# Kernel tuning notes

Hardware: AMD Instinct MI355X
Metric: run time of the kernel (lower is better)

## Reference

```python
import jax, jax.numpy as jnp
import numpy as np
from jax import lax

B, T, N, H, E = 128, 128, 49, 1024, 1024
EPS = 1e-6

def setup_inputs() -> dict:
    key = jax.random.key(0)
    ks = jax.random.split(key, 9)
    s = 0.02
    return {
        "X": jax.random.normal(ks[0], (B, T, E), jnp.float32),
        "G": jax.random.normal(ks[1], (2, B, H), jnp.float32),
        "L": jax.random.normal(ks[2], (B, N, H), jnp.float32),
        "W_ih0": jax.random.normal(ks[3], (3 * H, E), jnp.float32) * s,
        "W_hh0": jax.random.normal(ks[4], (3 * H, H), jnp.float32) * s,
        "W_ih1": jax.random.normal(ks[5], (3 * H, H), jnp.float32) * s,
        "W_hh1": jax.random.normal(ks[6], (3 * H, H), jnp.float32) * s,
        "W_lin": jax.random.normal(ks[7], (H, 2 * H), jnp.float32) * s,
        "a2": jnp.ones((H,), jnp.float32),
        "b2": jnp.zeros((H,), jnp.float32),
    }

def _gru_cell(x, h, W_ih, W_hh):
    # PyTorch GRUCell (bias=False): gates in order r, z, n
    gi = x @ W_ih.T  # [B, 3H]
    gh = h @ W_hh.T  # [B, 3H]
    i_r, i_z, i_n = jnp.split(gi, 3, axis=-1)
    h_r, h_z, h_n = jnp.split(gh, 3, axis=-1)
    r = jax.nn.sigmoid(i_r + h_r)
    z = jax.nn.sigmoid(i_z + h_z)
    n = jnp.tanh(i_n + r * h_n)
    return (1.0 - z) * n + z * h

def reference(X, G, L, W_ih0, W_hh0, W_ih1, W_hh1, W_lin, a2, b2):
    # NOTE: source attn() returns its input h (the bmm/softmax result is
    # discarded), so attention is dead code; dropout is eval-mode identity.
    def step(carry, xt):
        h0, h1_prev = carry            # each [B, H]
        h1 = _gru_cell(xt, h0, W_ih0, W_hh0)
        h2 = _gru_cell(h1, h1_prev, W_ih1, W_hh1)
        h_ = h2                        # drop (identity) + dead attn
        h0_new = jnp.tanh(jnp.concatenate([h0, h_], axis=1) @ W_lin.T)
        return (h0_new, h2), h0_new

    xs = jnp.swapaxes(X, 0, 1)         # [T, B, E]
    _, ys = lax.scan(step, (G[0], G[1]), xs)
    out = jnp.swapaxes(ys, 0, 1)       # [B, T, H]

    # LayerNorm with unbiased std and (std + eps) denominator (as in source)
    mean = out.mean(-1, keepdims=True)
    std = out.std(-1, ddof=1, keepdims=True)
    return a2 * (out - mean) / (std + EPS) + b2
```

## Files before the change

### kernel.cpp

```cpp
#include <hip/hip_runtime.h>
#include <hip/hip_bf16.h>

#define BB 128
#define TT 128
#define HH 1024
#define NWG 256
#define NT 512

typedef __bf16 bf16x8 __attribute__((ext_vector_type(8)));
typedef __bf16 bf16x4 __attribute__((ext_vector_type(4)));
typedef float  f32x4v __attribute__((ext_vector_type(4)));

#define MFMA16(a,b,c) __builtin_amdgcn_mfma_f32_16x16x32_bf16(a,b,c,0,0,0)

__device__ inline float fsig(float x) {
  x = fminf(fmaxf(x, -30.f), 30.f);
  return 1.f / (1.f + __expf(-x));
}
__device__ inline float ftanh(float x) {
  x = fminf(fmaxf(x, -15.f), 15.f);
  float e = __expf(2.f * x);
  return (e - 1.f) / (e + 1.f);
}
__device__ inline float bf2f(unsigned short u) {
  union { unsigned int i; float f; } c; c.i = (unsigned int)u << 16; return c.f;
}
__device__ inline void ucst16(__bf16* p, float v) {
  union { __bf16 b; unsigned short u; } c; c.b = (__bf16)v;
  __hip_atomic_store((unsigned short*)p, c.u, __ATOMIC_RELAXED, __HIP_MEMORY_SCOPE_AGENT);
}

#define SIGF(F) do { \
  __syncthreads(); \
  if (tid == 0) \
    __hip_atomic_store(&(F)[g], t + 1, __ATOMIC_RELAXED, __HIP_MEMORY_SCOPE_AGENT); \
} while (0)

__device__ inline void wf1(const int* F, int tgt, int tid, int lane) {
  if (tid < 64) {
    while (__hip_atomic_load(&F[lane], __ATOMIC_RELAXED, __HIP_MEMORY_SCOPE_AGENT) < tgt)
      __builtin_amdgcn_s_sleep(1);
    __builtin_amdgcn_fence(__ATOMIC_ACQUIRE, "agent");
  }
  __syncthreads();
  __builtin_amdgcn_sched_barrier(0);
}
__device__ inline void whalf(const int* F, int ch, int tgt, int tid, int lane) {
  if (tid < 64) {
    const int* P = F + ch * 32 + (lane & 31);
    while (__hip_atomic_load(P, __ATOMIC_RELAXED, __HIP_MEMORY_SCOPE_AGENT) < tgt)
      __builtin_amdgcn_s_sleep(1);
    __builtin_amdgcn_fence(__ATOMIC_ACQUIRE, "agent");
  }
  __syncthreads();
  __builtin_amdgcn_sched_barrier(0);
}

__device__ inline void stage_strip(char* dst, const float* src, int rstride, int tid) {
#pragma unroll
  for (int it = 0; it < 8; ++it) {
    int i = tid + it * NT;
    int rr = i >> 8;
    int c4 = i & 255;
    f32x4v v = *(const f32x4v*)(src + (size_t)rr * rstride + c4 * 4);
    bf16x4 o;
#pragma unroll
    for (int j = 0; j < 4; ++j) o[j] = (__bf16)v[j];
    *(bf16x4*)(dst + rr * 2048 + ((c4 * 8) ^ ((rr & 7) << 4))) = o;
  }
}

__device__ inline void stage_strip_b16(char* dst, const __bf16* src, int tid) {
#pragma unroll
  for (int it = 0; it < 8; ++it) {
    int i = tid + it * 256;
    int rr = i >> 7;
    int c8 = i & 127;
    bf16x8 v = *(const bf16x8*)(src + (size_t)rr * 1024 + c8 * 8);
    *(bf16x8*)(dst + rr * 2048 + ((c8 * 16) ^ ((rr & 7) << 4))) = v;
  }
}

template<int NS>
__device__ inline void gemm_half(const char* sm, const __bf16* __restrict__ A,
                                 int rowbase, int lane, int kb0, f32x4v (&acc)[NS]) {
  const int r = lane & 15, q = lane >> 4;
  const __bf16* Ap = A + (size_t)(rowbase + r) * 1024 + q * 8;
  bf16x8 a[16];
#pragma unroll
  for (int i = 0; i < 16; ++i) a[i] = *(const bf16x8*)(Ap + (kb0 + i) * 32);
  __builtin_amdgcn_sched_barrier(0);
  __builtin_amdgcn_s_setprio(1);
#pragma unroll
  for (int i = 0; i < 16; ++i) {
    const int kb = kb0 + i;
    const int byteo = (kb * 64 + q * 16) ^ ((r & 7) << 4);
#pragma unroll
    for (int s = 0; s < NS; ++s) {
      bf16x8 b = *(const bf16x8*)(sm + s * 32768 + r * 2048 + byteo);
      acc[s] = MFMA16(a[i], b, acc[s]);
    }
  }
  __builtin_amdgcn_s_setprio(0);
}

template<int NS>
__device__ inline void gemm_burst(const char* sm, const __bf16* __restrict__ A,
                                  int rowbase, int lane, f32x4v (&acc)[NS]) {
  const int r = lane & 15, q = lane >> 4;
  const __bf16* Ap = A + (size_t)(rowbase + r) * 1024 + q * 8;
  bf16x8 a[32];
#pragma unroll
  for (int kb = 0; kb < 32; ++kb) a[kb] = *(const bf16x8*)(Ap + kb * 32);
  __builtin_amdgcn_sched_barrier(0);
  __builtin_amdgcn_s_setprio(1);
#pragma unroll
  for (int kb = 0; kb < 32; ++kb) {
    const int byteo = (kb * 64 + q * 16) ^ ((r & 7) << 4);
#pragma unroll
    for (int s = 0; s < NS; ++s) {
      bf16x8 b = *(const bf16x8*)(sm + s * 32768 + r * 2048 + byteo);
      acc[s] = MFMA16(a[kb], b, acc[s]);
    }
  }
  __builtin_amdgcn_s_setprio(0);
}

__global__ void __launch_bounds__(NT, 2) gru_persist(
    const float* __restrict__ Whh0, const float* __restrict__ Wih1,
    const float* __restrict__ Whh1, const float* __restrict__ Wlin,
    const __bf16* __restrict__ gi0b, const float* __restrict__ G,
    __bf16* __restrict__ h0b, __bf16* __restrict__ h1b,
    __bf16* __restrict__ h2b, __bf16* __restrict__ gh1b,
    float* __restrict__ out, int* flags)
{
  __shared__ char sm[106496];
  float* h2s = (float*)(sm + 98304);
  const int tid = threadIdx.x, wg = blockIdx.x;
  const int wv = tid >> 6, lane = tid & 63;
  const int xcd = wg & 7;
  const int role = xcd >> 1;
  const int g = ((wg >> 3) << 1) | (xcd & 1);
  const int c0 = g * 16;
  const int r = lane & 15, q = lane >> 4;
  const bool gw = (wv < 4);

  if (role == 0) {
    stage_strip(sm,         Whh0 + (size_t)c0 * 1024,          1024, tid);
    stage_strip(sm + 32768, Whh0 + (size_t)(1024 + c0) * 1024, 1024, tid);
    stage_strip(sm + 65536, Whh0 + (size_t)(2048 + c0) * 1024, 1024, tid);
  } else if (role == 1) {
    stage_strip(sm,         Whh1 + (size_t)c0 * 1024,          1024, tid);
    stage_strip(sm + 32768, Whh1 + (size_t)(1024 + c0) * 1024, 1024, tid);
    stage_strip(sm + 65536, Whh1 + (size_t)(2048 + c0) * 1024, 1024, tid);
  } else if (role == 2) {
    stage_strip(sm,         Wih1 + (size_t)c0 * 1024,          1024, tid);
    stage_strip(sm + 32768, Wih1 + (size_t)(1024 + c0) * 1024, 1024, tid);
    stage_strip(sm + 65536, Wih1 + (size_t)(2048 + c0) * 1024, 1024, tid);
    for (int i = tid; i < 2048; i += NT) {
      int row = i >> 4, cc = i & 15;
      h2s[i] = G[131072 + row * 1024 + c0 + cc];
    }
  } else {
    stage_strip(sm,         Wlin + (size_t)c0 * 2048,        2048, tid);
    stage_strip(sm + 32768, Wlin + (size_t)c0 * 2048 + 1024, 2048, tid);
  }
  __syncthreads();

  int* F0h[2] = { flags + 0,   flags + 64 };
  int* F1h[2] = { flags + 128, flags + 192 };
  int* F2h[2] = { flags + 256, flags + 320 };
  int* F3h[2] = { flags + 384, flags + 448 };

  if (role == 0) {
    for (int t = 0; t < TT; ++t) {
      __bf16* h1bP = h1b + (size_t)(t & 1) * 131072;
#pragma unroll
      for (int h = 0; h < 2; ++h) {
        const int rowbase = h * 64 + wv * 16;
        f32x4v acc[3];
#pragma unroll
        for (int s = 0; s < 3; ++s) { f32x4v z = {0,0,0,0}; acc[s] = z; }
        whalf(F3h[h], 0, t, tid, lane);
        if (gw) gemm_half<3>(sm, h0b, rowbase, lane, 0, acc);
        whalf(F3h[h], 1, t, tid, lane);
        unsigned short ph[4], pgr[4], pgz[4], pgn[4];
        if (gw) {
#pragma unroll
          for (int gg = 0; gg < 4; ++gg) {
            int row = rowbase + q * 4 + gg;
            ph[gg] = *(const unsigned short*)(h0b + (size_t)row * 1024 + c0 + r);
            const unsigned short* gp =
                (const unsigned short*)(gi0b + ((size_t)t * 128 + row) * 3072 + c0 + r);
            pgr[gg] = gp[0]; pgz[gg] = gp[1024]; pgn[gg] = gp[2048];
          }
          gemm_half<3>(sm, h0b, rowbase, lane, 16, acc);
#pragma unroll
          for (int gg = 0; gg < 4; ++gg) {
            int row = rowbase + q * 4 + gg;
            float rv = fsig(bf2f(pgr[gg]) + acc[0][gg]);
            float zv = fsig(bf2f(pgz[gg]) + acc[1][gg]);
            float nv = ftanh(bf2f(pgn[gg]) + rv * acc[2][gg]);
            ucst16(h1bP + (size_t)row * 1024 + c0 + r, (1.f - zv) * nv + zv * bf2f(ph[gg]));
          }
        }
        SIGF(F0h[h]);
      }
    }
  } else if (role == 1) {
    for (int t = 0; t < TT; ++t) {
#pragma unroll
      for (int h = 0; h < 2; ++h) {
        wf1(F2h[h], t, tid, lane);
        if (gw) {
          const int rowbase = h * 64 + wv * 16;
          f32x4v acc[3];
#pragma unroll
          for (int s = 0; s < 3; ++s) { f32x4v z = {0,0,0,0}; acc[s] = z; }
          gemm_burst<3>(sm, h2b, rowbase, lane, acc);
#pragma unroll
          for (int gg = 0; gg < 4; ++gg) {
            size_t base = (size_t)(rowbase + q * 4 + gg) * 3072 + c0 + r;
            ucst16(gh1b + base,        acc[0][gg]);
            ucst16(gh1b + base + 1024, acc[1][gg]);
            ucst16(gh1b + base + 2048, acc[2][gg]);
          }
        }
        SIGF(F1h[h]);
      }
    }
  } else if (role == 2) {
    for (int t = 0; t < TT; ++t) {
      const __bf16* h1bP = h1b + (size_t)(t & 1) * 131072;
#pragma unroll
      for (int h = 0; h < 2; ++h) {
        const int rowbase = h * 64 + wv * 16;
        wf1(F1h[h], t + 1, tid, lane);
        unsigned short hg0[4], hg1[4], hg2[4];
        if (gw) {
#pragma unroll
          for (int gg = 0; gg < 4; ++gg) {
            int row = rowbase + q * 4 + gg;
            const unsigned short* hp = (const unsigned short*)(gh1b + (size_t)row * 3072 + c0 + r);
            hg0[gg] = hp[0]; hg1[gg] = hp[1024]; hg2[gg] = hp[2048];
          }
        }
        f32x4v acc[3];
#pragma unroll
        for (int s = 0; s < 3; ++s) { f32x4v z = {0,0,0,0}; acc[s] = z; }
        whalf(F0h[h], 0, t + 1, tid, lane);
        if (gw) gemm_half<3>(sm, h1bP, rowbase, lane, 0, acc);
        whalf(F0h[h], 1, t + 1, tid, lane);
        if (gw) {
          gemm_half<3>(sm, h1bP, rowbase, lane, 16, acc);
#pragma unroll
          for (int gg = 0; gg < 4; ++gg) {
            int row = rowbase + q * 4 + gg;
            float rv = fsig(acc[0][gg] + bf2f(hg0[gg]));
            float zv = fsig(acc[1][gg] + bf2f(hg1[gg]));
            float nv = ftanh(acc[2][gg] + rv * bf2f(hg2[gg]));
            float hp = h2s[row * 16 + r];
            float h2 = (1.f - zv) * nv + zv * hp;
            h2s[row * 16 + r] = h2;
            ucst16(h2b + (size_t)row * 1024 + c0 + r, h2);
          }
        }
        SIGF(F2h[h]);
      }
    }
  } else {
    for (int t = 0; t < TT; ++t) {
#pragma unroll
      for (int h = 0; h < 2; ++h) {
        const int rowbase = h * 64 + wv * 16;
        wf1(F3h[h], t, tid, lane);
        f32x4v accL[1];
        { f32x4v z = {0,0,0,0}; accL[0] = z; }
        if (gw) gemm_burst<1>(sm, h0b, rowbase, lane, accL);
        f32x4v accR[1];
        { f32x4v z = {0,0,0,0}; accR[0] = z; }
        whalf(F2h[h], 0, t + 1, tid, lane);
        if (gw) gemm_half<1>(sm + 32768, h2b, rowbase, lane, 0, accR);
        whalf(F2h[h], 1, t + 1, tid, lane);
        if (gw) {
          gemm_half<1>(sm + 32768, h2b, rowbase, lane, 16, accR);
#pragma unroll
          for (int gg = 0; gg < 4; ++gg) {
            int row = rowbase + q * 4 + gg;
            float v = ftanh(accL[0][gg] + accR[0][gg]);
            ucst16(h0b + (size_t)row * 1024 + c0 + r, v);
            out[((size_t)row * 128 + t) * 1024 + c0 + r] = v;
          }
        }
        SIGF(F3h[h]);
      }
    }
  }
}

__global__ void __launch_bounds__(256) gi0_kernel(const float* __restrict__ X,
                                                  const __bf16* __restrict__ Wih0b,
                                                  __bf16* __restrict__ gi0b) {
  __shared__ char sm[131072];
  const int tid = threadIdx.x, wv = tid >> 6, lane = tid & 63;
  const int bi = blockIdx.x;
  const int n = bi % 48, mg = bi / 48;
#pragma unroll
  for (int s = 0; s < 4; ++s)
    stage_strip_b16(sm + s * 32768, Wih0b + (size_t)(n * 64 + s * 16) * 1024, tid);
  __syncthreads();
  const int r = lane & 15, q = lane >> 4;
  for (int mi = mg * 4; mi < mg * 4 + 4; ++mi) {
    f32x4v acc[4][2];
#pragma unroll
    for (int s = 0; s < 4; ++s) { f32x4v z = {0,0,0,0}; acc[s][0] = z; acc[s][1] = z; }
    const float* Ap = X + ((size_t)mi * 128 + wv * 32 + r) * 1024 + q * 8;
#pragma unroll 4
    for (int kb = 0; kb < 32; ++kb) {
      f32x4v x0a = *(const f32x4v*)(Ap + kb * 32);
      f32x4v x0b = *(const f32x4v*)(Ap + kb * 32 + 4);
      f32x4v x1a = *(const f32x4v*)(Ap + 16384 + kb * 32);
      f32x4v x1b = *(const f32x4v*)(Ap + 16384 + kb * 32 + 4);
      bf16x8 a0, a1;
#pragma unroll
      for (int j = 0; j < 4; ++j) {
        a0[j] = (__bf16)x0a[j]; a0[4 + j] = (__bf16)x0b[j];
        a1[j] = (__bf16)x1a[j]; a1[4 + j] = (__bf16)x1b[j];
      }
      const int byteo = (kb * 64 + q * 16) ^ ((r & 7) << 4);
#pragma unroll
      for (int s = 0; s < 4; ++s) {
        bf16x8 b = *(const bf16x8*)(sm + s * 32768 + r * 2048 + byteo);
        acc[s][0] = MFMA16(a0, b, acc[s][0]);
        acc[s][1] = MFMA16(a1, b, acc[s][1]);
      }
    }
#pragma unroll
    for (int s = 0; s < 4; ++s)
#pragma unroll
      for (int mf = 0; mf < 2; ++mf)
#pragma unroll
        for (int gg = 0; gg < 4; ++gg) {
          int trow = wv * 32 + mf * 16 + q * 4 + gg;
          gi0b[((size_t)trow * 128 + mi) * 3072 + n * 64 + s * 16 + r] = (__bf16)acc[s][mf][gg];
        }
  }
}

__global__ void __launch_bounds__(256) prep3(const float* __restrict__ Wih0f,
                                             const float* __restrict__ G,
                                             __bf16* Wih0b,
                                             __bf16* h0b, __bf16* h2b, int* flags) {
  long c = (long)blockIdx.x * 256 + threadIdx.x;
  if (c < 786432) {
    f32x4v v = *(const f32x4v*)(Wih0f + c * 4);
    bf16x4 o;
#pragma unroll
    for (int j = 0; j < 4; ++j) o[j] = (__bf16)v[j];
    *(bf16x4*)(Wih0b + c * 4) = o;
  } else if (c < 786432 + 131072) {
    long i = c - 786432;
    h0b[i] = (__bf16)G[i];
  } else if (c < 786432 + 262144) {
    long i = c - 786432 - 131072;
    h2b[i] = (__bf16)G[131072 + i];
  } else if (c < 786432 + 262144 + 512) {
    flags[c - 786432 - 262144] = 0;
  }
}

__global__ void __launch_bounds__(256) ln_kernel(float* __restrict__ out,
                                                 const float* __restrict__ a2,
                                                 const float* __restrict__ b2) {
  int wv = threadIdx.x >> 6, lane = threadIdx.x & 63;
  size_t row = (size_t)blockIdx.x * 4 + wv;
  float* p = out + row * 1024;
  f32x4v v[4];
  float s = 0.f, ss = 0.f;
#pragma unroll
  for (int i = 0; i < 4; ++i) {
    v[i] = *(const f32x4v*)(p + (i * 64 + lane) * 4);
#pragma unroll
    for (int j = 0; j < 4; ++j) { s += v[i][j]; ss += v[i][j] * v[i][j]; }
  }
#pragma unroll
  for (int o = 32; o > 0; o >>= 1) { s += __shfl_xor(s, o); ss += __shfl_xor(ss, o); }
  float mean = s * (1.f / 1024.f);
  float var = (ss - 1024.f * mean * mean) * (1.f / 1023.f);
  var = fmaxf(var, 0.f);
  float inv = 1.f / (sqrtf(var) + 1e-6f);
#pragma unroll
  for (int i = 0; i < 4; ++i) {
    int c0 = (i * 64 + lane) * 4;
    f32x4v gA = *(const f32x4v*)(a2 + c0);
    f32x4v bo = *(const f32x4v*)(b2 + c0);
    f32x4v o;
#pragma unroll
    for (int j = 0; j < 4; ++j) o[j] = gA[j] * (v[i][j] - mean) * inv + bo[j];
    *(f32x4v*)(p + c0) = o;
  }
}

extern "C" void kernel_launch(void* const* d_in, const int* in_sizes, int n_in,
                              void* d_out, int out_size, void* d_ws, size_t ws_size,
                              hipStream_t stream) {
  const float* X    = (const float*)d_in[0];
  const float* G    = (const float*)d_in[1];
  const float* Wih0 = (const float*)d_in[3];
  const float* Whh0 = (const float*)d_in[4];
  const float* Wih1 = (const float*)d_in[5];
  const float* Whh1 = (const float*)d_in[6];
  const float* Wlin = (const float*)d_in[7];
  const float* a2   = (const float*)d_in[8];
  const float* b2   = (const float*)d_in[9];
  float* out = (float*)d_out;

  char* ws = (char*)d_ws;
  size_t off = 0;
  auto take = [&](size_t n) { char* p = ws + off; off += (n + 255) & ~(size_t)255; return p; };
  __bf16* Wih0b = (__bf16*)take((size_t)3072 * 1024 * 2);
  __bf16* gi0b  = (__bf16*)take((size_t)16384 * 3072 * 2);
  __bf16* gh1b  = (__bf16*)take((size_t)128 * 3072 * 2);
  __bf16* h0b   = (__bf16*)take((size_t)BB * HH * 2);
  __bf16* h1b   = (__bf16*)take((size_t)BB * HH * 2 * 2);
  __bf16* h2b   = (__bf16*)take((size_t)BB * HH * 2);
  int*    flags = (int*)take(512 * 4);
  if (off > ws_size) return;

  prep3<<<4099, 256, 0, stream>>>(Wih0, G, Wih0b, h0b, h2b, flags);
  gi0_kernel<<<1536, 256, 0, stream>>>(X, Wih0b, gi0b);
  gru_persist<<<NWG, NT, 0, stream>>>(Whh0, Wih1, Whh1, Wlin, gi0b, G,
                                      h0b, h1b, h2b, gh1b, out, flags);
  ln_kernel<<<4096, 256, 0, stream>>>(out, a2, b2);
}
```

Baseline: 4.196 ms.

## Replace workgroup-level half-batch flags with per-wave row-slice flags

Switches inter-workgroup synchronisation from per-workgroup flags covering 64-row halves, which needed __syncthreads and left half the waves idle, to per-wave flags covering each wave's own 16-row slice. All 8 waves now compute in a single pass per timestep, and each wave waits and signals on its own flags, so syncthreads barriers disappear from the recurrent loop. The intent is finer-grained dataflow that lets waves proceed as soon as their rows are ready. In exchange there are four times as many flags to poll and more atomic traffic, and correctness now depends on the per-wave s_waitcnt before each signal store.

After: 9.430 ms. 125% more time.

```diff
diff --git a/kernel.cpp b/kernel.cpp
--- a/kernel.cpp
+++ b/kernel.cpp
@@ -30,30 +30,34 @@
   __hip_atomic_store((unsigned short*)p, c.u, __ATOMIC_RELAXED, __HIP_MEMORY_SCOPE_AGENT);
 }
 
-#define SIGF(F) do { \
-  __syncthreads(); \
-  if (tid == 0) \
-    __hip_atomic_store(&(F)[g], t + 1, __ATOMIC_RELAXED, __HIP_MEMORY_SCOPE_AGENT); \
-} while (0)
-
-__device__ inline void wf1(const int* F, int tgt, int tid, int lane) {
-  if (tid < 64) {
-    while (__hip_atomic_load(&F[lane], __ATOMIC_RELAXED, __HIP_MEMORY_SCOPE_AGENT) < tgt)
+
+template<int NSLOT>
+__device__ inline void wvwait(const int* P, int tgt, int lane) {
+  if (lane < NSLOT) {
+    while (__hip_atomic_load(&P[lane], __ATOMIC_RELAXED, __HIP_MEMORY_SCOPE_AGENT) < tgt)
       __builtin_amdgcn_s_sleep(1);
-    __builtin_amdgcn_fence(__ATOMIC_ACQUIRE, "agent");
-  }
-  __syncthreads();
+  }
+  __builtin_amdgcn_fence(__ATOMIC_ACQUIRE, "agent");
   __builtin_amdgcn_sched_barrier(0);
 }
-__device__ inline void whalf(const int* F, int ch, int tgt, int tid, int lane) {
-  if (tid < 64) {
-    const int* P = F + ch * 32 + (lane & 31);
+__device__ inline void wvwait_pair(const int* A, const int* B2, int tgt, int lane) {
+  if (lane < 32) {
+    const int* P = A + lane;
     while (__hip_atomic_load(P, __ATOMIC_RELAXED, __HIP_MEMORY_SCOPE_AGENT) < tgt)
       __builtin_amdgcn_s_sleep(1);
-    __builtin_amdgcn_fence(__ATOMIC_ACQUIRE, "agent");
-  }
-  __syncthreads();
+  } else {
+    const int* P = B2 + (lane - 32) * 2;
+    while (__hip_atomic_load(P,     __ATOMIC_RELAXED, __HIP_MEMORY_SCOPE_AGENT) < tgt ||
+           __hip_atomic_load(P + 1, __ATOMIC_RELAXED, __HIP_MEMORY_SCOPE_AGENT) < tgt)
+      __builtin_amdgcn_s_sleep(1);
+  }
+  __builtin_amdgcn_fence(__ATOMIC_ACQUIRE, "agent");
   __builtin_amdgcn_sched_barrier(0);
+}
+__device__ inline void wvsig(int* slot, int val, int lane) {
+  asm volatile("s_waitcnt vmcnt(0)" ::: "memory");
+  if (lane == 0)
+    __hip_atomic_store(slot, val, __ATOMIC_RELAXED, __HIP_MEMORY_SCOPE_AGENT);
 }
 
 __device__ inline void stage_strip(char* dst, const float* src, int rstride, int tid) {
@@ -143,7 +147,7 @@
   const int g = ((wg >> 3) << 1) | (xcd & 1);
   const int c0 = g * 16;
   const int r = lane & 15, q = lane >> 4;
-  const bool gw = (wv < 4);
+  const int rowbase = wv * 16;
 
   if (role == 0) {
     stage_strip(sm,         Whh0 + (size_t)c0 * 1024,          1024, tid);
@@ -167,133 +171,121 @@
   }
   __syncthreads();
 
-  int* F0h[2] = { flags + 0,   flags + 64 };
-  int* F1h[2] = { flags + 128, flags + 192 };
-  int* F2h[2] = { flags + 256, flags + 320 };
-  int* F3h[2] = { flags + 384, flags + 448 };
+  int* F0 = flags;
+  int* F1 = flags + 512;
+  int* F2 = flags + 1024;
+  int* F3 = flags + 1536;
 
   if (role == 0) {
+    const int* Fw = F3 + wv * 64;
+    int*       Fs = F0 + wv * 64 + g;
     for (int t = 0; t < TT; ++t) {
       __bf16* h1bP = h1b + (size_t)(t & 1) * 131072;
-#pragma unroll
-      for (int h = 0; h < 2; ++h) {
-        const int rowbase = h * 64 + wv * 16;
-        f32x4v acc[3];
-#pragma unroll
-        for (int s = 0; s < 3; ++s) { f32x4v z = {0,0,0,0}; acc[s] = z; }
-        whalf(F3h[h], 0, t, tid, lane);
-        if (gw) gemm_half<3>(sm, h0b, rowbase, lane, 0, acc);
-        whalf(F3h[h], 1, t, tid, lane);
-        unsigned short ph[4], pgr[4], pgz[4], pgn[4];
-        if (gw) {
-#pragma unroll
-          for (int gg = 0; gg < 4; ++gg) {
-            int row = rowbase + q * 4 + gg;
-            ph[gg] = *(const unsigned short*)(h0b + (size_t)row * 1024 + c0 + r);
-            const unsigned short* gp =
-                (const unsigned short*)(gi0b + ((size_t)t * 128 + row) * 3072 + c0 + r);
-            pgr[gg] = gp[0]; pgz[gg] = gp[1024]; pgn[gg] = gp[2048];
-          }
-          gemm_half<3>(sm, h0b, rowbase, lane, 16, acc);
-#pragma unroll
-          for (int gg = 0; gg < 4; ++gg) {
-            int row = rowbase + q * 4 + gg;
-            float rv = fsig(bf2f(pgr[gg]) + acc[0][gg]);
-            float zv = fsig(bf2f(pgz[gg]) + acc[1][gg]);
-            float nv = ftanh(bf2f(pgn[gg]) + rv * acc[2][gg]);
-            ucst16(h1bP + (size_t)row * 1024 + c0 + r, (1.f - zv) * nv + zv * bf2f(ph[gg]));
-          }
-        }
-        SIGF(F0h[h]);
-      }
+      unsigned short pgr[4], pgz[4], pgn[4];
+#pragma unroll
+      for (int gg = 0; gg < 4; ++gg) {
+        int row = rowbase + q * 4 + gg;
+        const unsigned short* gp =
+            (const unsigned short*)(gi0b + ((size_t)t * 128 + row) * 3072 + c0 + r);
+        pgr[gg] = gp[0]; pgz[gg] = gp[1024]; pgn[gg] = gp[2048];
+      }
+      f32x4v acc[3];
+#pragma unroll
+      for (int s = 0; s < 3; ++s) { f32x4v z = {0,0,0,0}; acc[s] = z; }
+      wvwait<32>(Fw, t, lane);
+      gemm_half<3>(sm, h0b, rowbase, lane, 0, acc);
+      wvwait<32>(Fw + 32, t, lane);
+      unsigned short ph[4];
+#pragma unroll
+      for (int gg = 0; gg < 4; ++gg)
+        ph[gg] = *(const unsigned short*)(h0b + (size_t)(rowbase + q * 4 + gg) * 1024 + c0 + r);
+      gemm_half<3>(sm, h0b, rowbase, lane, 16, acc);
+#pragma unroll
+      for (int gg = 0; gg < 4; ++gg) {
+        int row = rowbase + q * 4 + gg;
+        float rv = fsig(bf2f(pgr[gg]) + acc[0][gg]);
+        float zv = fsig(bf2f(pgz[gg]) + acc[1][gg]);
+        float nv = ftanh(bf2f(pgn[gg]) + rv * acc[2][gg]);
+        ucst16(h1bP + (size_t)row * 1024 + c0 + r, (1.f - zv) * nv + zv * bf2f(ph[gg]));
+      }
+      wvsig(Fs, t + 1, lane);
     }
   } else if (role == 1) {
+    const int* Fw = F2 + wv * 64;
+    int*       Fs = F1 + wv * 64 + g;
     for (int t = 0; t < TT; ++t) {
-#pragma unroll
-      for (int h = 0; h < 2; ++h) {
-        wf1(F2h[h], t, tid, lane);
-        if (gw) {
-          const int rowbase = h * 64 + wv * 16;
-          f32x4v acc[3];
-#pragma unroll
-          for (int s = 0; s < 3; ++s) { f32x4v z = {0,0,0,0}; acc[s] = z; }
-          gemm_burst<3>(sm, h2b, rowbase, lane, acc);
-#pragma unroll
-          for (int gg = 0; gg < 4; ++gg) {
-            size_t base = (size_t)(rowbase + q * 4 + gg) * 3072 + c0 + r;
-            ucst16(gh1b + base,        acc[0][gg]);
-            ucst16(gh1b + base + 1024, acc[1][gg]);
-            ucst16(gh1b + base + 2048, acc[2][gg]);
-          }
-        }
-        SIGF(F1h[h]);
-      }
+      wvwait<64>(Fw, t, lane);
+      f32x4v acc[3];
+#pragma unroll
+      for (int s = 0; s < 3; ++s) { f32x4v z = {0,0,0,0}; acc[s] = z; }
+      gemm_burst<3>(sm, h2b, rowbase, lane, acc);
+#pragma unroll
+      for (int gg = 0; gg < 4; ++gg) {
+        size_t base = (size_t)(rowbase + q * 4 + gg) * 3072 + c0 + r;
+        ucst16(gh1b + base,        acc[0][gg]);
+        ucst16(gh1b + base + 1024, acc[1][gg]);
+        ucst16(gh1b + base + 2048, acc[2][gg]);
+      }
+      wvsig(Fs, t + 1, lane);
     }
   } else if (role == 2) {
+    const int* FwA = F1 + wv * 64 + g;
+    const int* FwB = F0 + wv * 64;
+    const int* FwC = F1 + wv * 64;
+    int*       Fs  = F2 + wv * 64 + g;
     for (int t = 0; t < TT; ++t) {
       const __bf16* h1bP = h1b + (size_t)(t & 1) * 131072;
-#pragma unroll
-      for (int h = 0; h < 2; ++h) {
-        const int rowbase = h * 64 + wv * 16;
-        wf1(F1h[h], t + 1, tid, lane);
-        unsigned short hg0[4], hg1[4], hg2[4];
-        if (gw) {
-#pragma unroll
-          for (int gg = 0; gg < 4; ++gg) {
-            int row = rowbase + q * 4 + gg;
-            const unsigned short* hp = (const unsigned short*)(gh1b + (size_t)row * 3072 + c0 + r);
-            hg0[gg] = hp[0]; hg1[gg] = hp[1024]; hg2[gg] = hp[2048];
-          }
-        }
-        f32x4v acc[3];
-#pragma unroll
-        for (int s = 0; s < 3; ++s) { f32x4v z = {0,0,0,0}; acc[s] = z; }
-        whalf(F0h[h], 0, t + 1, tid, lane);
-        if (gw) gemm_half<3>(sm, h1bP, rowbase, lane, 0, acc);
-        whalf(F0h[h], 1, t + 1, tid, lane);
-        if (gw) {
-          gemm_half<3>(sm, h1bP, rowbase, lane, 16, acc);
-#pragma unroll
-          for (int gg = 0; gg < 4; ++gg) {
-            int row = rowbase + q * 4 + gg;
-            float rv = fsig(acc[0][gg] + bf2f(hg0[gg]));
-            float zv = fsig(acc[1][gg] + bf2f(hg1[gg]));
-            float nv = ftanh(acc[2][gg] + rv * bf2f(hg2[gg]));
-            float hp = h2s[row * 16 + r];
-            float h2 = (1.f - zv) * nv + zv * hp;
-            h2s[row * 16 + r] = h2;
-            ucst16(h2b + (size_t)row * 1024 + c0 + r, h2);
-          }
-        }
-        SIGF(F2h[h]);
-      }
+      wvwait<1>(FwA, t + 1, lane);
+      unsigned short hg0[4], hg1[4], hg2[4];
+#pragma unroll
+      for (int gg = 0; gg < 4; ++gg) {
+        const unsigned short* hp =
+            (const unsigned short*)(gh1b + (size_t)(rowbase + q * 4 + gg) * 3072 + c0 + r);
+        hg0[gg] = hp[0]; hg1[gg] = hp[1024]; hg2[gg] = hp[2048];
+      }
+      f32x4v acc[3];
+#pragma unroll
+      for (int s = 0; s < 3; ++s) { f32x4v z = {0,0,0,0}; acc[s] = z; }
+      wvwait<32>(FwB, t + 1, lane);
+      gemm_half<3>(sm, h1bP, rowbase, lane, 0, acc);
+      wvwait_pair(FwB + 32, FwC, t + 1, lane);
+      gemm_half<3>(sm, h1bP, rowbase, lane, 16, acc);
+#pragma unroll
+      for (int gg = 0; gg < 4; ++gg) {
+        int row = rowbase + q * 4 + gg;
+        float rv = fsig(acc[0][gg] + bf2f(hg0[gg]));
+        float zv = fsig(acc[1][gg] + bf2f(hg1[gg]));
+        float nv = ftanh(acc[2][gg] + rv * bf2f(hg2[gg]));
+        float hp = h2s[row * 16 + r];
+        float h2 = (1.f - zv) * nv + zv * hp;
+        h2s[row * 16 + r] = h2;
+        ucst16(h2b + (size_t)row * 1024 + c0 + r, h2);
+      }
+      wvsig(Fs, t + 1, lane);
     }
   } else {
+    const int* FwOwn = F3 + wv * 64;
+    const int* FwC   = F2 + wv * 64;
+    int*       Fs    = F3 + wv * 64 + g;
     for (int t = 0; t < TT; ++t) {
-#pragma unroll
-      for (int h = 0; h < 2; ++h) {
-        const int rowbase = h * 64 + wv * 16;
-        wf1(F3h[h], t, tid, lane);
-        f32x4v accL[1];
-        { f32x4v z = {0,0,0,0}; accL[0] = z; }
-        if (gw) gemm_burst<1>(sm, h0b, rowbase, lane, accL);
-        f32x4v accR[1];
-        { f32x4v z = {0,0,0,0}; accR[0] = z; }
-        whalf(F2h[h], 0, t + 1, tid, lane);
-        if (gw) gemm_half<1>(sm + 32768, h2b, rowbase, lane, 0, accR);
-        whalf(F2h[h], 1, t + 1, tid, lane);
-        if (gw) {
-          gemm_half<1>(sm + 32768, h2b, rowbase, lane, 16, accR);
-#pragma unroll
-          for (int gg = 0; gg < 4; ++gg) {
-            int row = rowbase + q * 4 + gg;
-            float v = ftanh(accL[0][gg] + accR[0][gg]);
-            ucst16(h0b + (size_t)row * 1024 + c0 + r, v);
-            out[((size_t)row * 128 + t) * 1024 + c0 + r] = v;
-          }
-        }
-        SIGF(F3h[h]);
-      }
+      wvwait<64>(FwOwn, t, lane);
+      f32x4v accL[1];
+      { f32x4v z = {0,0,0,0}; accL[0] = z; }
+      gemm_burst<1>(sm, h0b, rowbase, lane, accL);
+      f32x4v accR[1];
+      { f32x4v z = {0,0,0,0}; accR[0] = z; }
+      wvwait<32>(FwC, t + 1, lane);
+      gemm_half<1>(sm + 32768, h2b, rowbase, lane, 0, accR);
+      wvwait<32>(FwC + 32, t + 1, lane);
+      gemm_half<1>(sm + 32768, h2b, rowbase, lane, 16, accR);
+#pragma unroll
+      for (int gg = 0; gg < 4; ++gg) {
+        int row = rowbase + q * 4 + gg;
+        float v = ftanh(accL[0][gg] + accR[0][gg]);
+        ucst16(h0b + (size_t)row * 1024 + c0 + r, v);
+        out[((size_t)row * 128 + t) * 1024 + c0 + r] = v;
+      }
+      wvsig(Fs, t + 1, lane);
     }
   }
 }
@@ -364,7 +356,7 @@
   } else if (c < 786432 + 262144) {
     long i = c - 786432 - 131072;
     h2b[i] = (__bf16)G[131072 + i];
-  } else if (c < 786432 + 262144 + 512) {
+  } else if (c < 786432 + 262144 + 2048) {
     flags[c - 786432 - 262144] = 0;
   }
 }
@@ -424,10 +416,10 @@
   __bf16* h0b   = (__bf16*)take((size_t)BB * HH * 2);
   __bf16* h1b   = (__bf16*)take((size_t)BB * HH * 2 * 2);
   __bf16* h2b   = (__bf16*)take((size_t)BB * HH * 2);
-  int*    flags = (int*)take(512 * 4);
+  int*    flags = (int*)take(2048 * 4);
   if (off > ws_size) return;
 
-  prep3<<<4099, 256, 0, stream>>>(Wih0, G, Wih0b, h0b, h2b, flags);
+  prep3<<<4104, 256, 0, stream>>>(Wih0, G, Wih0b, h0b, h2b, flags);
   gi0_kernel<<<1536, 256, 0, stream>>>(X, Wih0b, gi0b);
   gru_persist<<<NWG, NT, 0, stream>>>(Whh0, Wih1, Whh1, Wlin, gi0b, G,
                                       h0b, h1b, h2b, gh1b, out, flags);
```
